# Performance work log

Measured on AMD Instinct MI355X. Metric: run time of the kernel, lower is better.

Reference implementation:

```python
import jax, jax.numpy as jnp
import numpy as np

N_NODES = 100000
IN_DIM = 64
HID = 64
N_EDGES = 1600000
EPS = 1e-5
SLOPE = 0.01  # F.leaky_relu default


def _glorot(key, shape):
    fan_in, fan_out = shape[1], shape[0]
    lim = jnp.sqrt(6.0 / (fan_in + fan_out))
    return jax.random.uniform(key, shape, jnp.float32, -lim, lim)


def setup_inputs() -> dict:
    key = jax.random.key(0)
    ks = jax.random.split(key, 8)
    x = jax.random.normal(ks[0], (N_NODES, IN_DIM), jnp.float32)
    src = jax.random.randint(ks[1], (N_EDGES,), 0, N_NODES, jnp.int32)
    dst = jax.random.randint(ks[2], (N_EDGES,), 0, N_NODES, jnp.int32)
    edge_index = jnp.stack([src, dst])  # [2, E]
    return {
        "x": x,
        "edge_index": edge_index,
        "W_self1": _glorot(ks[3], (HID, IN_DIM)),
        "W_neigh1": _glorot(ks[4], (HID, IN_DIM)),
        "b1": jnp.zeros((HID,), jnp.float32),
        "gamma1": jnp.ones((HID,), jnp.float32),
        "beta1": jnp.zeros((HID,), jnp.float32),
        "W_self2": _glorot(ks[5], (HID, HID)),
        "W_neigh2": _glorot(ks[6], (HID, HID)),
        "b2": jnp.zeros((HID,), jnp.float32),
        "gamma2": jnp.ones((HID,), jnp.float32),
        "beta2": jnp.zeros((HID,), jnp.float32),
    }


def _sage_mean(h, src, dst, W_self, W_neigh, b):
    # neighbor mean aggregation: mean of src features at each dst node
    msg_sum = jax.ops.segment_sum(h[src], dst, num_segments=N_NODES)  # [N, d]
    deg = jax.ops.segment_sum(jnp.ones_like(dst, jnp.float32), dst, num_segments=N_NODES)
    h_neigh = msg_sum / jnp.maximum(deg, 1.0)[:, None]  # isolated nodes -> 0
    return h @ W_self.T + h_neigh @ W_neigh.T + b


def _bn(h, gamma, beta):
    mu = jnp.mean(h, axis=0)
    var = jnp.mean(jnp.square(h - mu), axis=0)
    return (h - mu) * jax.lax.rsqrt(var + EPS) * gamma + beta


def reference(x, edge_index, W_self1, W_neigh1, b1, gamma1, beta1,
              W_self2, W_neigh2, b2, gamma2, beta2):
    src, dst = edge_index[0], edge_index[1]
    h = _sage_mean(x, src, dst, W_self1, W_neigh1, b1)
    h = jax.nn.leaky_relu(_bn(h, gamma1, beta1), SLOPE)
    h = _sage_mean(h, src, dst, W_self2, W_neigh2, b2)
    h = jax.nn.leaky_relu(_bn(h, gamma2, beta2), SLOPE)
    return h
```

## Files before the change

### kernel.cpp

```cpp
#include <hip/hip_runtime.h>

#define EPS 1e-5f
#define SLOPE 0.01f

typedef short bf16x8 __attribute__((ext_vector_type(8)));
typedef float f32x4 __attribute__((ext_vector_type(4)));

static __device__ __forceinline__ unsigned short f2bf(float f) {
  unsigned u = __float_as_uint(f);
  unsigned r = (u + 0x7FFFu + ((u >> 16) & 1u)) >> 16;
  return (unsigned short)r;
}
#define BFLO(u) __uint_as_float((u) << 16)
#define BFHI(u) __uint_as_float((u) & 0xFFFF0000u)


__global__ __launch_bounds__(1024) void hist_cvt_kernel(
    const int* __restrict__ dst, int* __restrict__ hist, int E, int NB,
    int histBlocks, const float* __restrict__ x, unsigned short* __restrict__ xb,
    int total4) {
  extern __shared__ int lh[];
  if ((int)blockIdx.x < histBlocks) {
    for (int i = threadIdx.x; i < NB; i += blockDim.x) lh[i] = 0;
    __syncthreads();
    int E4 = E >> 2;
    int stride = histBlocks * blockDim.x;
    const int4* d4 = (const int4*)dst;
    for (int i = blockIdx.x * blockDim.x + threadIdx.x; i < E4; i += stride) {
      int4 d = d4[i];
      atomicAdd(&lh[((unsigned)d.x) >> 8], 1);
      atomicAdd(&lh[((unsigned)d.y) >> 8], 1);
      atomicAdd(&lh[((unsigned)d.z) >> 8], 1);
      atomicAdd(&lh[((unsigned)d.w) >> 8], 1);
    }
    if (blockIdx.x == 0) {
      for (int i = (E4 << 2) + threadIdx.x; i < E; i += blockDim.x)
        atomicAdd(&lh[((unsigned)dst[i]) >> 8], 1);
    }
    __syncthreads();
    for (int b = threadIdx.x; b < NB; b += blockDim.x)
      hist[(size_t)b * histBlocks + blockIdx.x] = lh[b];
  } else {
    int cb = blockIdx.x - histBlocks;
    int stride = (gridDim.x - histBlocks) * blockDim.x;
    for (int i = cb * blockDim.x + threadIdx.x; i < total4; i += stride) {
      float4 v = reinterpret_cast<const float4*>(x)[i];
      ushort4 o;
      o.x = f2bf(v.x); o.y = f2bf(v.y); o.z = f2bf(v.z); o.w = f2bf(v.w);
      reinterpret_cast<ushort4*>(xb)[i] = o;
    }
  }
}

__global__ void scan_blk(const int* in, int* out, int* bsum, int n) {
  __shared__ int s[256];
  int i = blockIdx.x * 256 + threadIdx.x;
  int v = (i < n) ? in[i] : 0;
  s[threadIdx.x] = v;
  __syncthreads();
  for (int off = 1; off < 256; off <<= 1) {
    int t = (threadIdx.x >= off) ? s[threadIdx.x - off] : 0;
    __syncthreads();
    s[threadIdx.x] += t;
    __syncthreads();
  }
  if (i < n) out[i] = s[threadIdx.x] - v;
  if (threadIdx.x == 255) bsum[blockIdx.x] = s[255];
}

__global__ void scan_top(int* bsum, int nb) {
  __shared__ int s[512];
  int tid = threadIdx.x;
  int v = (tid < nb) ? bsum[tid] : 0;
  s[tid] = v;
  __syncthreads();
  for (int off = 1; off < 512; off <<= 1) {
    int t = (tid >= off) ? s[tid - off] : 0;
    __syncthreads();
    s[tid] += t;
    __syncthreads();
  }
  if (tid < nb) bsum[tid] = s[tid] - v;
}

__global__ __launch_bounds__(1024) void scatter_kernel(
    const int* __restrict__ src, const int* __restrict__ dst,
    const int* __restrict__ histS, const int* __restrict__ bsum,
    unsigned* __restrict__ binned, int E, int NB) {
  extern __shared__ int cur[];
  for (int b = threadIdx.x; b < NB; b += blockDim.x)
    cur[b] = histS[(size_t)b * gridDim.x + blockIdx.x] + bsum[b];
  __syncthreads();
  int E4 = E >> 2;
  int stride = gridDim.x * blockDim.x;
  const int4* d4 = (const int4*)dst;
  const int4* s4 = (const int4*)src;
  for (int i = blockIdx.x * blockDim.x + threadIdx.x; i < E4; i += stride) {
    int4 d = d4[i];
    int4 s = s4[i];
    int b0 = ((unsigned)d.x) >> 8;
    binned[atomicAdd(&cur[b0], 1)] = (unsigned)s.x | (((unsigned)d.x & 255u) << 20);
    int b1 = ((unsigned)d.y) >> 8;
    binned[atomicAdd(&cur[b1], 1)] = (unsigned)s.y | (((unsigned)d.y & 255u) << 20);
    int b2 = ((unsigned)d.z) >> 8;
    binned[atomicAdd(&cur[b2], 1)] = (unsigned)s.z | (((unsigned)d.z & 255u) << 20);
    int b3 = ((unsigned)d.w) >> 8;
    binned[atomicAdd(&cur[b3], 1)] = (unsigned)s.w | (((unsigned)d.w & 255u) << 20);
  }
  if (blockIdx.x == 0) {
    for (int i = (E4 << 2) + threadIdx.x; i < E; i += blockDim.x) {
      int d = dst[i];
      int b = ((unsigned)d) >> 8;
      binned[atomicAdd(&cur[b], 1)] = (unsigned)src[i] | (((unsigned)d & 255u) << 20);
    }
  }
}

__global__ __launch_bounds__(256) void fine_kernel(
    const unsigned* __restrict__ binned, const int* __restrict__ histS,
    const int* __restrict__ bsum,
    int* __restrict__ rowptr, int* __restrict__ col, int E, int NB, int NBLKB, int N) {
  __shared__ int ldeg[256];
  __shared__ int lcur[256];
  __shared__ int ss[256];
  int b = blockIdx.x;
  int tid = threadIdx.x;
  int seg_s = histS[(size_t)b * NBLKB] + bsum[b];
  int seg_e = (b + 1 < NB) ? (histS[(size_t)(b + 1) * NBLKB] + bsum[b + 1]) : E;
  ldeg[tid] = 0;
  __syncthreads();
  for (int i = seg_s + tid; i < seg_e; i += 256)
    atomicAdd(&ldeg[(binned[i] >> 20) & 255u], 1);
  __syncthreads();
  int d = ldeg[tid];
  ss[tid] = d;
  __syncthreads();
  for (int off = 1; off < 256; off <<= 1) {
    int t = (tid >= off) ? ss[tid - off] : 0;
    __syncthreads();
    ss[tid] += t;
    __syncthreads();
  }
  int base = seg_s + ss[tid] - d;
  lcur[tid] = base;
  int node = (b << 8) + tid;
  if (node < N) rowptr[node] = base;
  if (b == NB - 1 && tid == 0) rowptr[N] = E;
  __syncthreads();
  for (int i = seg_s + tid; i < seg_e; i += 256) {
    unsigned v = binned[i];
    int pos = atomicAdd(&lcur[(v >> 20) & 255u], 1);
    col[pos] = (int)(v & 0xFFFFFu);
  }
}


__global__ __launch_bounds__(256) void agg_kernel(
    const unsigned short* __restrict__ hb, const int* __restrict__ rowptr,
    const int* __restrict__ col, unsigned short* __restrict__ hm, int n) {
  int t = blockIdx.x * 256 + threadIdx.x;
  int node = t >> 3;
  int fo = (t & 7) * 8;
  if (node >= n) return;
  int beg = rowptr[node];
  int end = rowptr[node + 1];
  float s0 = 0.f, s1 = 0.f, s2 = 0.f, s3 = 0.f;
  float s4 = 0.f, s5 = 0.f, s6 = 0.f, s7 = 0.f;
  int e = beg;
  for (; e + 4 <= end; e += 4) {
    int i0 = col[e], i1 = col[e + 1], i2 = col[e + 2], i3 = col[e + 3];
    uint4 u0 = *reinterpret_cast<const uint4*>(&hb[(size_t)i0 * 64 + fo]);
    uint4 u1 = *reinterpret_cast<const uint4*>(&hb[(size_t)i1 * 64 + fo]);
    uint4 u2 = *reinterpret_cast<const uint4*>(&hb[(size_t)i2 * 64 + fo]);
    uint4 u3 = *reinterpret_cast<const uint4*>(&hb[(size_t)i3 * 64 + fo]);
    s0 += BFLO(u0.x) + BFLO(u1.x) + BFLO(u2.x) + BFLO(u3.x);
    s1 += BFHI(u0.x) + BFHI(u1.x) + BFHI(u2.x) + BFHI(u3.x);
    s2 += BFLO(u0.y) + BFLO(u1.y) + BFLO(u2.y) + BFLO(u3.y);
    s3 += BFHI(u0.y) + BFHI(u1.y) + BFHI(u2.y) + BFHI(u3.y);
    s4 += BFLO(u0.z) + BFLO(u1.z) + BFLO(u2.z) + BFLO(u3.z);
    s5 += BFHI(u0.z) + BFHI(u1.z) + BFHI(u2.z) + BFHI(u3.z);
    s6 += BFLO(u0.w) + BFLO(u1.w) + BFLO(u2.w) + BFLO(u3.w);
    s7 += BFHI(u0.w) + BFHI(u1.w) + BFHI(u2.w) + BFHI(u3.w);
  }
  for (; e < end; ++e) {
    uint4 u = *reinterpret_cast<const uint4*>(&hb[(size_t)col[e] * 64 + fo]);
    s0 += BFLO(u.x); s1 += BFHI(u.x);
    s2 += BFLO(u.y); s3 += BFHI(u.y);
    s4 += BFLO(u.z); s5 += BFHI(u.z);
    s6 += BFLO(u.w); s7 += BFHI(u.w);
  }
  int deg = end - beg;
  float inv = 1.0f / (float)(deg > 0 ? deg : 1);
  uint4 o;
  o.x = (unsigned)f2bf(s0 * inv) | ((unsigned)f2bf(s1 * inv) << 16);
  o.y = (unsigned)f2bf(s2 * inv) | ((unsigned)f2bf(s3 * inv) << 16);
  o.z = (unsigned)f2bf(s4 * inv) | ((unsigned)f2bf(s5 * inv) << 16);
  o.w = (unsigned)f2bf(s6 * inv) | ((unsigned)f2bf(s7 * inv) << 16);
  *reinterpret_cast<uint4*>(&hm[(size_t)node * 64 + fo]) = o;
}


__global__ __launch_bounds__(256) void gemm_stream(
    const unsigned short* __restrict__ A0,
    const unsigned short* __restrict__ A1,
    const float* __restrict__ Wself, const float* __restrict__ Wneigh,
    const float* __restrict__ bias,
    unsigned short* __restrict__ zb, float* __restrict__ partial, int n, int ntiles) {
  int tid = threadIdx.x;
  int lane = tid & 63;
  int w = tid >> 6;
  int l15 = lane & 15;
  int g = lane >> 4;

  bf16x8 B[4][4];
  #pragma unroll
  for (int t = 0; t < 4; ++t) {
    #pragma unroll
    for (int s = 0; s < 4; ++s) {
      const float* base = (s < 2 ? Wself : Wneigh) + (t * 16 + l15) * 64 + (s & 1) * 32 + g * 8;
      float4 w0 = *reinterpret_cast<const float4*>(base);
      float4 w1 = *reinterpret_cast<const float4*>(base + 4);
      bf16x8 b;
      b[0] = (short)f2bf(w0.x); b[1] = (short)f2bf(w0.y);
      b[2] = (short)f2bf(w0.z); b[3] = (short)f2bf(w0.w);
      b[4] = (short)f2bf(w1.x); b[5] = (short)f2bf(w1.y);
      b[6] = (short)f2bf(w1.z); b[7] = (short)f2bf(w1.w);
      B[t][s] = b;
    }
  }
  float bv[4];
  #pragma unroll
  for (int t = 0; t < 4; ++t) bv[t] = bias[t * 16 + l15];

  float ps[4] = {0.f, 0.f, 0.f, 0.f};
  float pq[4] = {0.f, 0.f, 0.f, 0.f};

  int nw = gridDim.x * 4;
  for (int tile = blockIdx.x * 4 + w; tile < ntiles; tile += nw) {
    int r0 = tile * 16 + l15;
    uint4 a[4];
    if (r0 < n) {
      const uint4* pa0 = reinterpret_cast<const uint4*>(A0 + (size_t)r0 * 64);
      const uint4* pa1 = reinterpret_cast<const uint4*>(A1 + (size_t)r0 * 64);
      a[0] = pa0[g]; a[1] = pa0[4 + g]; a[2] = pa1[g]; a[3] = pa1[4 + g];
    } else {
      a[0] = a[1] = a[2] = a[3] = make_uint4(0u, 0u, 0u, 0u);
    }
    f32x4 acc[4] = {};
    #pragma unroll
    for (int s = 0; s < 4; ++s) {
      bf16x8 af = *reinterpret_cast<bf16x8*>(&a[s]);
      #pragma unroll
      for (int t = 0; t < 4; ++t)
        acc[t] = __builtin_amdgcn_mfma_f32_16x16x32_bf16(af, B[t][s], acc[t], 0, 0, 0);
    }
    #pragma unroll
    for (int t = 0; t < 4; ++t) {
      #pragma unroll
      for (int i = 0; i < 4; ++i) {
        int gr = tile * 16 + g * 4 + i;
        if (gr < n) {
          float v = acc[t][i] + bv[t];
          zb[(size_t)gr * 64 + t * 16 + l15] = f2bf(v);
          ps[t] += v;
          pq[t] += v * v;
        }
      }
    }
  }

  #pragma unroll
  for (int t = 0; t < 4; ++t) {
    ps[t] += __shfl_xor(ps[t], 16); ps[t] += __shfl_xor(ps[t], 32);
    pq[t] += __shfl_xor(pq[t], 16); pq[t] += __shfl_xor(pq[t], 32);
  }
  __shared__ float sred[128];
  if (tid < 128) sred[tid] = 0.f;
  __syncthreads();
  if (lane < 16) {
    #pragma unroll
    for (int t = 0; t < 4; ++t) {
      atomicAdd(&sred[t * 16 + l15], ps[t]);
      atomicAdd(&sred[64 + t * 16 + l15], pq[t]);
    }
  }
  __syncthreads();
  if (tid < 128) partial[(size_t)blockIdx.x * 128 + tid] = sred[tid];
}

__global__ __launch_bounds__(256) void reduce_coef(
    const float* __restrict__ partial, const float* __restrict__ gamma,
    const float* __restrict__ beta, float* __restrict__ coef, int nblk, float invN) {
  int f = blockIdx.x;
  float s = 0.f, q = 0.f;
  for (int j = threadIdx.x; j < nblk; j += 256) {
    s += partial[(size_t)j * 128 + f];
    q += partial[(size_t)j * 128 + 64 + f];
  }
  #pragma unroll
  for (int o = 1; o < 64; o <<= 1) {
    s += __shfl_xor(s, o);
    q += __shfl_xor(q, o);
  }
  __shared__ float rs[4], rq[4];
  if ((threadIdx.x & 63) == 0) {
    rs[threadIdx.x >> 6] = s;
    rq[threadIdx.x >> 6] = q;
  }
  __syncthreads();
  if (threadIdx.x == 0) {
    float S = rs[0] + rs[1] + rs[2] + rs[3];
    float Q = rq[0] + rq[1] + rq[2] + rq[3];
    float mu = S * invN;
    float var = Q * invN - mu * mu;
    float sc = rsqrtf(var + EPS) * gamma[f];
    coef[f] = sc;
    coef[64 + f] = beta[f] - mu * sc;
  }
}


__global__ void bn_bf16_kernel(const unsigned short* __restrict__ zb,
                               const float* __restrict__ coef,
                               unsigned short* __restrict__ out, int n) {
  __shared__ float sc[64];
  __shared__ float sh[64];
  if (threadIdx.x < 64) {
    sc[threadIdx.x] = coef[threadIdx.x];
    sh[threadIdx.x] = coef[64 + threadIdx.x];
  }
  __syncthreads();
  int total = n * 16;
  int stride = gridDim.x * blockDim.x;
  for (int idx = blockIdx.x * blockDim.x + threadIdx.x; idx < total; idx += stride) {
    int f0 = (idx & 15) * 4;
    uint2 u = reinterpret_cast<const uint2*>(zb)[idx];
    float t;
    ushort4 o;
    t = BFLO(u.x) * sc[f0 + 0] + sh[f0 + 0]; o.x = f2bf(t > 0.f ? t : SLOPE * t);
    t = BFHI(u.x) * sc[f0 + 1] + sh[f0 + 1]; o.y = f2bf(t > 0.f ? t : SLOPE * t);
    t = BFLO(u.y) * sc[f0 + 2] + sh[f0 + 2]; o.z = f2bf(t > 0.f ? t : SLOPE * t);
    t = BFHI(u.y) * sc[f0 + 3] + sh[f0 + 3]; o.w = f2bf(t > 0.f ? t : SLOPE * t);
    reinterpret_cast<ushort4*>(out)[idx] = o;
  }
}

__global__ void bn_f32_kernel(const unsigned short* __restrict__ zb,
                              const float* __restrict__ coef,
                              float* __restrict__ out, int n) {
  __shared__ float sc[64];
  __shared__ float sh[64];
  if (threadIdx.x < 64) {
    sc[threadIdx.x] = coef[threadIdx.x];
    sh[threadIdx.x] = coef[64 + threadIdx.x];
  }
  __syncthreads();
  int total = n * 16;
  int stride = gridDim.x * blockDim.x;
  for (int idx = blockIdx.x * blockDim.x + threadIdx.x; idx < total; idx += stride) {
    int f0 = (idx & 15) * 4;
    uint2 u = reinterpret_cast<const uint2*>(zb)[idx];
    float4 o;
    float t;
    t = BFLO(u.x) * sc[f0 + 0] + sh[f0 + 0]; o.x = t > 0.f ? t : SLOPE * t;
    t = BFHI(u.x) * sc[f0 + 1] + sh[f0 + 1]; o.y = t > 0.f ? t : SLOPE * t;
    t = BFLO(u.y) * sc[f0 + 2] + sh[f0 + 2]; o.z = t > 0.f ? t : SLOPE * t;
    t = BFHI(u.y) * sc[f0 + 3] + sh[f0 + 3]; o.w = t > 0.f ? t : SLOPE * t;
    reinterpret_cast<float4*>(out)[idx] = o;
  }
}


extern "C" void kernel_launch(void* const* d_in, const int* in_sizes, int n_in,
                              void* d_out, int out_size, void* d_ws, size_t ws_size,
                              hipStream_t stream) {
  const float* x  = (const float*)d_in[0];
  const int* ei   = (const int*)d_in[1];
  const float* Ws1 = (const float*)d_in[2];
  const float* Wn1 = (const float*)d_in[3];
  const float* b1  = (const float*)d_in[4];
  const float* g1  = (const float*)d_in[5];
  const float* be1 = (const float*)d_in[6];
  const float* Ws2 = (const float*)d_in[7];
  const float* Wn2 = (const float*)d_in[8];
  const float* b2  = (const float*)d_in[9];
  const float* g2  = (const float*)d_in[10];
  const float* be2 = (const float*)d_in[11];
  float* out = (float*)d_out;

  int N = in_sizes[0] / 64;
  int E = in_sizes[1] / 2;
  const int* src = ei;
  const int* dst = ei + E;

  int NB = (N + 255) >> 8;
  const int NBLKB = 256;
  int M = NB * NBLKB;

  int ntiles = (N + 15) / 16;
  int gblk = (ntiles + 7) / 8;

  char* ws = (char*)d_ws;
  float* coef1 = (float*)ws;
  float* coef2 = coef1 + 128;
  size_t off = 1024;
  auto take = [&](size_t bytes) {
    void* p = ws + off;
    off = (off + bytes + 255) & ~(size_t)255;
    return p;
  };
  int* hist   = (int*)take((size_t)M * 4);
  int* bsum   = (int*)take(512 * 4);
  int* rowptr = (int*)take((size_t)(N + 1) * 4);
  unsigned* binned = (unsigned*)take((size_t)E * 4);
  int* col    = (int*)take((size_t)E * 4);
  unsigned short* xb  = (unsigned short*)take((size_t)N * 64 * 2);
  unsigned short* hmb = (unsigned short*)take((size_t)N * 64 * 2);
  unsigned short* h1b = (unsigned short*)take((size_t)N * 64 * 2);
  unsigned short* zb  = (unsigned short*)take((size_t)N * 64 * 2);
  float* partial = (float*)take((size_t)gblk * 128 * 4);

  hist_cvt_kernel<<<NBLKB + 128, 1024, NB * 4, stream>>>(dst, hist, E, NB, NBLKB,
                                                         x, xb, N * 16);
  int nb1 = (M + 255) / 256;
  scan_blk<<<nb1, 256, 0, stream>>>(hist, hist, bsum, M);
  scan_top<<<1, 512, 0, stream>>>(bsum, nb1);
  scatter_kernel<<<NBLKB, 1024, NB * 4, stream>>>(src, dst, hist, bsum, binned, E, NB);
  fine_kernel<<<NB, 256, 0, stream>>>(binned, hist, bsum, rowptr, col, E, NB, NBLKB, N);

  int ab = (N * 8 + 255) / 256;
  float invN = 1.0f / (float)N;

  agg_kernel<<<ab, 256, 0, stream>>>(xb, rowptr, col, hmb, N);
  gemm_stream<<<gblk, 256, 0, stream>>>(xb, hmb, Ws1, Wn1, b1, zb, partial, N, ntiles);
  reduce_coef<<<64, 256, 0, stream>>>(partial, g1, be1, coef1, gblk, invN);
  bn_bf16_kernel<<<2048, 256, 0, stream>>>(zb, coef1, h1b, N);

  agg_kernel<<<ab, 256, 0, stream>>>(h1b, rowptr, col, hmb, N);
  gemm_stream<<<gblk, 256, 0, stream>>>(h1b, hmb, Ws2, Wn2, b2, zb, partial, N, ntiles);
  reduce_coef<<<64, 256, 0, stream>>>(partial, g2, be2, coef2, gblk, invN);
  bn_f32_kernel<<<2048, 256, 0, stream>>>(zb, coef2, out, N);
}
```

Before: 174.8 us.

## Fuse neighbor aggregation into GEMM via shared-memory staging per 64-row tile

Merges the mean-aggregation kernel into the MFMA GEMM kernel. Each block of 256 threads now aggregates 64 nodes into an fp32 shared tile and converts it to bf16 MFMA operands directly. This removes the hmb intermediate buffer's write and reread plus one launch per layer. In exchange there are far more blocks (one per 64 rows), each reloading and converting the weights. The GEMM loses its persistent-tile loop, and the partial-stats array grows, which adds work to reduce_coef.

```diff
diff --git a/kernel.cpp b/kernel.cpp
--- a/kernel.cpp
+++ b/kernel.cpp
@@ -155,58 +155,63 @@
 }
 
 
-__global__ __launch_bounds__(256) void agg_kernel(
-    const unsigned short* __restrict__ hb, const int* __restrict__ rowptr,
-    const int* __restrict__ col, unsigned short* __restrict__ hm, int n) {
-  int t = blockIdx.x * 256 + threadIdx.x;
-  int node = t >> 3;
-  int fo = (t & 7) * 8;
-  if (node >= n) return;
-  int beg = rowptr[node];
-  int end = rowptr[node + 1];
-  float s0 = 0.f, s1 = 0.f, s2 = 0.f, s3 = 0.f;
-  float s4 = 0.f, s5 = 0.f, s6 = 0.f, s7 = 0.f;
-  int e = beg;
-  for (; e + 4 <= end; e += 4) {
-    int i0 = col[e], i1 = col[e + 1], i2 = col[e + 2], i3 = col[e + 3];
-    uint4 u0 = *reinterpret_cast<const uint4*>(&hb[(size_t)i0 * 64 + fo]);
-    uint4 u1 = *reinterpret_cast<const uint4*>(&hb[(size_t)i1 * 64 + fo]);
-    uint4 u2 = *reinterpret_cast<const uint4*>(&hb[(size_t)i2 * 64 + fo]);
-    uint4 u3 = *reinterpret_cast<const uint4*>(&hb[(size_t)i3 * 64 + fo]);
-    s0 += BFLO(u0.x) + BFLO(u1.x) + BFLO(u2.x) + BFLO(u3.x);
-    s1 += BFHI(u0.x) + BFHI(u1.x) + BFHI(u2.x) + BFHI(u3.x);
-    s2 += BFLO(u0.y) + BFLO(u1.y) + BFLO(u2.y) + BFLO(u3.y);
-    s3 += BFHI(u0.y) + BFHI(u1.y) + BFHI(u2.y) + BFHI(u3.y);
-    s4 += BFLO(u0.z) + BFLO(u1.z) + BFLO(u2.z) + BFLO(u3.z);
-    s5 += BFHI(u0.z) + BFHI(u1.z) + BFHI(u2.z) + BFHI(u3.z);
-    s6 += BFLO(u0.w) + BFLO(u1.w) + BFLO(u2.w) + BFLO(u3.w);
-    s7 += BFHI(u0.w) + BFHI(u1.w) + BFHI(u2.w) + BFHI(u3.w);
-  }
-  for (; e < end; ++e) {
-    uint4 u = *reinterpret_cast<const uint4*>(&hb[(size_t)col[e] * 64 + fo]);
-    s0 += BFLO(u.x); s1 += BFHI(u.x);
-    s2 += BFLO(u.y); s3 += BFHI(u.y);
-    s4 += BFLO(u.z); s5 += BFHI(u.z);
-    s6 += BFLO(u.w); s7 += BFHI(u.w);
-  }
-  int deg = end - beg;
-  float inv = 1.0f / (float)(deg > 0 ? deg : 1);
-  uint4 o;
-  o.x = (unsigned)f2bf(s0 * inv) | ((unsigned)f2bf(s1 * inv) << 16);
-  o.y = (unsigned)f2bf(s2 * inv) | ((unsigned)f2bf(s3 * inv) << 16);
-  o.z = (unsigned)f2bf(s4 * inv) | ((unsigned)f2bf(s5 * inv) << 16);
-  o.w = (unsigned)f2bf(s6 * inv) | ((unsigned)f2bf(s7 * inv) << 16);
-  *reinterpret_cast<uint4*>(&hm[(size_t)node * 64 + fo]) = o;
-}
-
-
-__global__ __launch_bounds__(256) void gemm_stream(
-    const unsigned short* __restrict__ A0,
-    const unsigned short* __restrict__ A1,
+#define XLD 65
+
+__global__ __launch_bounds__(256, 4) void fused_layer(
+    const unsigned short* __restrict__ hb,
+    const int* __restrict__ rowptr, const int* __restrict__ col,
     const float* __restrict__ Wself, const float* __restrict__ Wneigh,
     const float* __restrict__ bias,
-    unsigned short* __restrict__ zb, float* __restrict__ partial, int n, int ntiles) {
+    unsigned short* __restrict__ zb, float* __restrict__ partial, int n) {
+  __shared__ float X[64 * XLD];
+  __shared__ float sred[128];
   int tid = threadIdx.x;
+  int rowbase = blockIdx.x * 64;
+
+  int si = tid & 7;
+  int gi = tid >> 3;
+  #pragma unroll
+  for (int b = 0; b < 2; ++b) {
+    int node = rowbase + b * 32 + gi;
+    float a0 = 0.f, a1 = 0.f, a2 = 0.f, a3 = 0.f;
+    float a4 = 0.f, a5 = 0.f, a6 = 0.f, a7 = 0.f;
+    int deg = 0;
+    if (node < n) {
+      int beg = rowptr[node];
+      int end = rowptr[node + 1];
+      deg = end - beg;
+      int e = beg;
+      for (; e + 4 <= end; e += 4) {
+        int i0 = col[e], i1 = col[e + 1], i2 = col[e + 2], i3 = col[e + 3];
+        uint4 u0 = *reinterpret_cast<const uint4*>(&hb[(size_t)i0 * 64 + si * 8]);
+        uint4 u1 = *reinterpret_cast<const uint4*>(&hb[(size_t)i1 * 64 + si * 8]);
+        uint4 u2 = *reinterpret_cast<const uint4*>(&hb[(size_t)i2 * 64 + si * 8]);
+        uint4 u3 = *reinterpret_cast<const uint4*>(&hb[(size_t)i3 * 64 + si * 8]);
+        a0 += BFLO(u0.x) + BFLO(u1.x) + BFLO(u2.x) + BFLO(u3.x);
+        a1 += BFHI(u0.x) + BFHI(u1.x) + BFHI(u2.x) + BFHI(u3.x);
+        a2 += BFLO(u0.y) + BFLO(u1.y) + BFLO(u2.y) + BFLO(u3.y);
+        a3 += BFHI(u0.y) + BFHI(u1.y) + BFHI(u2.y) + BFHI(u3.y);
+        a4 += BFLO(u0.z) + BFLO(u1.z) + BFLO(u2.z) + BFLO(u3.z);
+        a5 += BFHI(u0.z) + BFHI(u1.z) + BFHI(u2.z) + BFHI(u3.z);
+        a6 += BFLO(u0.w) + BFLO(u1.w) + BFLO(u2.w) + BFLO(u3.w);
+        a7 += BFHI(u0.w) + BFHI(u1.w) + BFHI(u2.w) + BFHI(u3.w);
+      }
+      for (; e < end; ++e) {
+        uint4 u = *reinterpret_cast<const uint4*>(&hb[(size_t)col[e] * 64 + si * 8]);
+        a0 += BFLO(u.x); a1 += BFHI(u.x);
+        a2 += BFLO(u.y); a3 += BFHI(u.y);
+        a4 += BFLO(u.z); a5 += BFHI(u.z);
+        a6 += BFLO(u.w); a7 += BFHI(u.w);
+      }
+    }
+    float inv = 1.0f / (float)(deg > 0 ? deg : 1);
+    float* xr = &X[(b * 32 + gi) * XLD + si * 8];
+    xr[0] = a0 * inv; xr[1] = a1 * inv; xr[2] = a2 * inv; xr[3] = a3 * inv;
+    xr[4] = a4 * inv; xr[5] = a5 * inv; xr[6] = a6 * inv; xr[7] = a7 * inv;
+  }
+  if (tid < 128) sred[tid] = 0.f;
+  __syncthreads();
+
   int lane = tid & 63;
   int w = tid >> 6;
   int l15 = lane & 15;
@@ -220,51 +225,59 @@
       const float* base = (s < 2 ? Wself : Wneigh) + (t * 16 + l15) * 64 + (s & 1) * 32 + g * 8;
       float4 w0 = *reinterpret_cast<const float4*>(base);
       float4 w1 = *reinterpret_cast<const float4*>(base + 4);
-      bf16x8 b;
-      b[0] = (short)f2bf(w0.x); b[1] = (short)f2bf(w0.y);
-      b[2] = (short)f2bf(w0.z); b[3] = (short)f2bf(w0.w);
-      b[4] = (short)f2bf(w1.x); b[5] = (short)f2bf(w1.y);
-      b[6] = (short)f2bf(w1.z); b[7] = (short)f2bf(w1.w);
-      B[t][s] = b;
+      bf16x8 bb;
+      bb[0] = (short)f2bf(w0.x); bb[1] = (short)f2bf(w0.y);
+      bb[2] = (short)f2bf(w0.z); bb[3] = (short)f2bf(w0.w);
+      bb[4] = (short)f2bf(w1.x); bb[5] = (short)f2bf(w1.y);
+      bb[6] = (short)f2bf(w1.z); bb[7] = (short)f2bf(w1.w);
+      B[t][s] = bb;
     }
   }
   float bv[4];
   #pragma unroll
   for (int t = 0; t < 4; ++t) bv[t] = bias[t * 16 + l15];
+
+  int r0 = rowbase + w * 16 + l15;
+  uint4 a0[2];
+  if (r0 < n) {
+    const uint4* pa0 = reinterpret_cast<const uint4*>(hb + (size_t)r0 * 64);
+    a0[0] = pa0[g]; a0[1] = pa0[4 + g];
+  } else {
+    a0[0] = a0[1] = make_uint4(0u, 0u, 0u, 0u);
+  }
+  const float* xr = &X[(w * 16 + l15) * XLD];
+  bf16x8 a1[2];
+  #pragma unroll
+  for (int h = 0; h < 2; ++h) {
+    const float* p = xr + h * 32 + g * 8;
+    bf16x8 v;
+    #pragma unroll
+    for (int j = 0; j < 8; ++j) v[j] = (short)f2bf(p[j]);
+    a1[h] = v;
+  }
+
+  f32x4 acc[4] = {};
+  #pragma unroll
+  for (int s = 0; s < 4; ++s) {
+    bf16x8 af = (s < 2) ? *reinterpret_cast<bf16x8*>(&a0[s])
+                        : a1[s - 2];
+    #pragma unroll
+    for (int t = 0; t < 4; ++t)
+      acc[t] = __builtin_amdgcn_mfma_f32_16x16x32_bf16(af, B[t][s], acc[t], 0, 0, 0);
+  }
 
   float ps[4] = {0.f, 0.f, 0.f, 0.f};
   float pq[4] = {0.f, 0.f, 0.f, 0.f};
-
-  int nw = gridDim.x * 4;
-  for (int tile = blockIdx.x * 4 + w; tile < ntiles; tile += nw) {
-    int r0 = tile * 16 + l15;
-    uint4 a[4];
-    if (r0 < n) {
-      const uint4* pa0 = reinterpret_cast<const uint4*>(A0 + (size_t)r0 * 64);
-      const uint4* pa1 = reinterpret_cast<const uint4*>(A1 + (size_t)r0 * 64);
-      a[0] = pa0[g]; a[1] = pa0[4 + g]; a[2] = pa1[g]; a[3] = pa1[4 + g];
-    } else {
-      a[0] = a[1] = a[2] = a[3] = make_uint4(0u, 0u, 0u, 0u);
-    }
-    f32x4 acc[4] = {};
+  #pragma unroll
+  for (int t = 0; t < 4; ++t) {
     #pragma unroll
-    for (int s = 0; s < 4; ++s) {
-      bf16x8 af = *reinterpret_cast<bf16x8*>(&a[s]);
-      #pragma unroll
-      for (int t = 0; t < 4; ++t)
-        acc[t] = __builtin_amdgcn_mfma_f32_16x16x32_bf16(af, B[t][s], acc[t], 0, 0, 0);
-    }
-    #pragma unroll
-    for (int t = 0; t < 4; ++t) {
-      #pragma unroll
-      for (int i = 0; i < 4; ++i) {
-        int gr = tile * 16 + g * 4 + i;
-        if (gr < n) {
-          float v = acc[t][i] + bv[t];
-          zb[(size_t)gr * 64 + t * 16 + l15] = f2bf(v);
-          ps[t] += v;
-          pq[t] += v * v;
-        }
+    for (int i = 0; i < 4; ++i) {
+      int gr = rowbase + w * 16 + g * 4 + i;
+      if (gr < n) {
+        float v = acc[t][i] + bv[t];
+        zb[(size_t)gr * 64 + t * 16 + l15] = f2bf(v);
+        ps[t] += v;
+        pq[t] += v * v;
       }
     }
   }
@@ -274,9 +287,6 @@
     ps[t] += __shfl_xor(ps[t], 16); ps[t] += __shfl_xor(ps[t], 32);
     pq[t] += __shfl_xor(pq[t], 16); pq[t] += __shfl_xor(pq[t], 32);
   }
-  __shared__ float sred[128];
-  if (tid < 128) sred[tid] = 0.f;
-  __syncthreads();
   if (lane < 16) {
     #pragma unroll
     for (int t = 0; t < 4; ++t) {
@@ -397,8 +407,7 @@
   const int NBLKB = 256;
   int M = NB * NBLKB;
 
-  int ntiles = (N + 15) / 16;
-  int gblk = (ntiles + 7) / 8;
+  int NSUPER = (N + 63) / 64;
 
   char* ws = (char*)d_ws;
   float* coef1 = (float*)ws;
@@ -415,10 +424,9 @@
   unsigned* binned = (unsigned*)take((size_t)E * 4);
   int* col    = (int*)take((size_t)E * 4);
   unsigned short* xb  = (unsigned short*)take((size_t)N * 64 * 2);
-  unsigned short* hmb = (unsigned short*)take((size_t)N * 64 * 2);
   unsigned short* h1b = (unsigned short*)take((size_t)N * 64 * 2);
   unsigned short* zb  = (unsigned short*)take((size_t)N * 64 * 2);
-  float* partial = (float*)take((size_t)gblk * 128 * 4);
+  float* partial = (float*)take((size_t)NSUPER * 128 * 4);
 
   hist_cvt_kernel<<<NBLKB + 128, 1024, NB * 4, stream>>>(dst, hist, E, NB, NBLKB,
                                                          x, xb, N * 16);
@@ -428,16 +436,13 @@
   scatter_kernel<<<NBLKB, 1024, NB * 4, stream>>>(src, dst, hist, bsum, binned, E, NB);
   fine_kernel<<<NB, 256, 0, stream>>>(binned, hist, bsum, rowptr, col, E, NB, NBLKB, N);
 
-  int ab = (N * 8 + 255) / 256;
   float invN = 1.0f / (float)N;
 
-  agg_kernel<<<ab, 256, 0, stream>>>(xb, rowptr, col, hmb, N);
-  gemm_stream<<<gblk, 256, 0, stream>>>(xb, hmb, Ws1, Wn1, b1, zb, partial, N, ntiles);
-  reduce_coef<<<64, 256, 0, stream>>>(partial, g1, be1, coef1, gblk, invN);
+  fused_layer<<<NSUPER, 256, 0, stream>>>(xb, rowptr, col, Ws1, Wn1, b1, zb, partial, N);
+  reduce_coef<<<64, 256, 0, stream>>>(partial, g1, be1, coef1, NSUPER, invN);
   bn_bf16_kernel<<<2048, 256, 0, stream>>>(zb, coef1, h1b, N);
 
-  agg_kernel<<<ab, 256, 0, stream>>>(h1b, rowptr, col, hmb, N);
-  gemm_stream<<<gblk, 256, 0, stream>>>(h1b, hmb, Ws2, Wn2, b2, zb, partial, N, ntiles);
-  reduce_coef<<<64, 256, 0, stream>>>(partial, g2, be2, coef2, gblk, invN);
+  fused_layer<<<NSUPER, 256, 0, stream>>>(h1b, rowptr, col, Ws2, Wn2, b2, zb, partial, N);
+  reduce_coef<<<64, 256, 0, stream>>>(partial, g2, be2, coef2, NSUPER, invN);
   bn_f32_kernel<<<2048, 256, 0, stream>>>(zb, coef2, out, N);
 }
```

Measured after the change: 244.3 us. 39.8% more time.

## Fuse layer-1 batchnorm and leaky ReLU into layer-2 aggregation and GEMM

Applied to the files above, without the earlier changes.

Removes the standalone bf16 batchnorm pass for layer 1 and its intermediate h1b buffer. The layer-1 BN scale/shift and leaky ReLU are now applied on the fly to the raw pre-BN activations: per gathered neighbour row in the aggregation kernel, and per self row in the GEMM kernel. This saves one full read and write of the N×64 activation array plus a kernel launch. In exchange the aggregation does extra FMA and select work for every edge. The GEMM also reads and writes zb in place, which conflicts with its __restrict__ qualifiers. An occupancy hint (launch_bounds 256,8) is also added to the aggregation kernel.

```diff
diff --git a/kernel.cpp b/kernel.cpp
--- a/kernel.cpp
+++ b/kernel.cpp
@@ -155,17 +155,43 @@
 }
 
 
-__global__ __launch_bounds__(256) void agg_kernel(
+template <bool BN>
+__global__ __launch_bounds__(256, 8) void agg_kernel(
     const unsigned short* __restrict__ hb, const int* __restrict__ rowptr,
-    const int* __restrict__ col, unsigned short* __restrict__ hm, int n) {
+    const int* __restrict__ col, const float* __restrict__ coef,
+    unsigned short* __restrict__ hm, int n) {
   int t = blockIdx.x * 256 + threadIdx.x;
   int node = t >> 3;
   int fo = (t & 7) * 8;
   if (node >= n) return;
+  float scr[8], shr[8];
+  if (BN) {
+    #pragma unroll
+    for (int j = 0; j < 8; ++j) {
+      scr[j] = coef[fo + j];
+      shr[j] = coef[64 + fo + j];
+    }
+  }
   int beg = rowptr[node];
   int end = rowptr[node + 1];
   float s0 = 0.f, s1 = 0.f, s2 = 0.f, s3 = 0.f;
   float s4 = 0.f, s5 = 0.f, s6 = 0.f, s7 = 0.f;
+  auto acc1 = [&](uint4 u) {
+    float v0 = BFLO(u.x), v1 = BFHI(u.x), v2 = BFLO(u.y), v3 = BFHI(u.y);
+    float v4 = BFLO(u.z), v5 = BFHI(u.z), v6 = BFLO(u.w), v7 = BFHI(u.w);
+    if (BN) {
+      v0 = v0 * scr[0] + shr[0]; v0 = v0 > 0.f ? v0 : SLOPE * v0;
+      v1 = v1 * scr[1] + shr[1]; v1 = v1 > 0.f ? v1 : SLOPE * v1;
+      v2 = v2 * scr[2] + shr[2]; v2 = v2 > 0.f ? v2 : SLOPE * v2;
+      v3 = v3 * scr[3] + shr[3]; v3 = v3 > 0.f ? v3 : SLOPE * v3;
+      v4 = v4 * scr[4] + shr[4]; v4 = v4 > 0.f ? v4 : SLOPE * v4;
+      v5 = v5 * scr[5] + shr[5]; v5 = v5 > 0.f ? v5 : SLOPE * v5;
+      v6 = v6 * scr[6] + shr[6]; v6 = v6 > 0.f ? v6 : SLOPE * v6;
+      v7 = v7 * scr[7] + shr[7]; v7 = v7 > 0.f ? v7 : SLOPE * v7;
+    }
+    s0 += v0; s1 += v1; s2 += v2; s3 += v3;
+    s4 += v4; s5 += v5; s6 += v6; s7 += v7;
+  };
   int e = beg;
   for (; e + 4 <= end; e += 4) {
     int i0 = col[e], i1 = col[e + 1], i2 = col[e + 2], i3 = col[e + 3];
@@ -173,21 +199,11 @@
     uint4 u1 = *reinterpret_cast<const uint4*>(&hb[(size_t)i1 * 64 + fo]);
     uint4 u2 = *reinterpret_cast<const uint4*>(&hb[(size_t)i2 * 64 + fo]);
     uint4 u3 = *reinterpret_cast<const uint4*>(&hb[(size_t)i3 * 64 + fo]);
-    s0 += BFLO(u0.x) + BFLO(u1.x) + BFLO(u2.x) + BFLO(u3.x);
-    s1 += BFHI(u0.x) + BFHI(u1.x) + BFHI(u2.x) + BFHI(u3.x);
-    s2 += BFLO(u0.y) + BFLO(u1.y) + BFLO(u2.y) + BFLO(u3.y);
-    s3 += BFHI(u0.y) + BFHI(u1.y) + BFHI(u2.y) + BFHI(u3.y);
-    s4 += BFLO(u0.z) + BFLO(u1.z) + BFLO(u2.z) + BFLO(u3.z);
-    s5 += BFHI(u0.z) + BFHI(u1.z) + BFHI(u2.z) + BFHI(u3.z);
-    s6 += BFLO(u0.w) + BFLO(u1.w) + BFLO(u2.w) + BFLO(u3.w);
-    s7 += BFHI(u0.w) + BFHI(u1.w) + BFHI(u2.w) + BFHI(u3.w);
+    acc1(u0); acc1(u1); acc1(u2); acc1(u3);
   }
   for (; e < end; ++e) {
     uint4 u = *reinterpret_cast<const uint4*>(&hb[(size_t)col[e] * 64 + fo]);
-    s0 += BFLO(u.x); s1 += BFHI(u.x);
-    s2 += BFLO(u.y); s3 += BFHI(u.y);
-    s4 += BFLO(u.z); s5 += BFHI(u.z);
-    s6 += BFLO(u.w); s7 += BFHI(u.w);
+    acc1(u);
   }
   int deg = end - beg;
   float inv = 1.0f / (float)(deg > 0 ? deg : 1);
@@ -200,11 +216,12 @@
 }
 
 
+template <bool BN>
 __global__ __launch_bounds__(256) void gemm_stream(
     const unsigned short* __restrict__ A0,
     const unsigned short* __restrict__ A1,
     const float* __restrict__ Wself, const float* __restrict__ Wneigh,
-    const float* __restrict__ bias,
+    const float* __restrict__ bias, const float* __restrict__ coef,
     unsigned short* __restrict__ zb, float* __restrict__ partial, int n, int ntiles) {
   int tid = threadIdx.x;
   int lane = tid & 63;
@@ -232,6 +249,18 @@
   #pragma unroll
   for (int t = 0; t < 4; ++t) bv[t] = bias[t * 16 + l15];
 
+  float scA[2][8], shA[2][8];
+  if (BN) {
+    #pragma unroll
+    for (int h = 0; h < 2; ++h) {
+      #pragma unroll
+      for (int j = 0; j < 8; ++j) {
+        scA[h][j] = coef[h * 32 + g * 8 + j];
+        shA[h][j] = coef[64 + h * 32 + g * 8 + j];
+      }
+    }
+  }
+
   float ps[4] = {0.f, 0.f, 0.f, 0.f};
   float pq[4] = {0.f, 0.f, 0.f, 0.f};
 
@@ -245,6 +274,28 @@
       a[0] = pa0[g]; a[1] = pa0[4 + g]; a[2] = pa1[g]; a[3] = pa1[4 + g];
     } else {
       a[0] = a[1] = a[2] = a[3] = make_uint4(0u, 0u, 0u, 0u);
+    }
+    if (BN) {
+      #pragma unroll
+      for (int h = 0; h < 2; ++h) {
+        uint4 u = a[h];
+        float v0 = BFLO(u.x), v1 = BFHI(u.x), v2 = BFLO(u.y), v3 = BFHI(u.y);
+        float v4 = BFLO(u.z), v5 = BFHI(u.z), v6 = BFLO(u.w), v7 = BFHI(u.w);
+        v0 = v0 * scA[h][0] + shA[h][0]; v0 = v0 > 0.f ? v0 : SLOPE * v0;
+        v1 = v1 * scA[h][1] + shA[h][1]; v1 = v1 > 0.f ? v1 : SLOPE * v1;
+        v2 = v2 * scA[h][2] + shA[h][2]; v2 = v2 > 0.f ? v2 : SLOPE * v2;
+        v3 = v3 * scA[h][3] + shA[h][3]; v3 = v3 > 0.f ? v3 : SLOPE * v3;
+        v4 = v4 * scA[h][4] + shA[h][4]; v4 = v4 > 0.f ? v4 : SLOPE * v4;
+        v5 = v5 * scA[h][5] + shA[h][5]; v5 = v5 > 0.f ? v5 : SLOPE * v5;
+        v6 = v6 * scA[h][6] + shA[h][6]; v6 = v6 > 0.f ? v6 : SLOPE * v6;
+        v7 = v7 * scA[h][7] + shA[h][7]; v7 = v7 > 0.f ? v7 : SLOPE * v7;
+        uint4 r;
+        r.x = (unsigned)f2bf(v0) | ((unsigned)f2bf(v1) << 16);
+        r.y = (unsigned)f2bf(v2) | ((unsigned)f2bf(v3) << 16);
+        r.z = (unsigned)f2bf(v4) | ((unsigned)f2bf(v5) << 16);
+        r.w = (unsigned)f2bf(v6) | ((unsigned)f2bf(v7) << 16);
+        a[h] = r;
+      }
     }
     f32x4 acc[4] = {};
     #pragma unroll
@@ -319,31 +370,6 @@
   }
 }
 
-
-__global__ void bn_bf16_kernel(const unsigned short* __restrict__ zb,
-                               const float* __restrict__ coef,
-                               unsigned short* __restrict__ out, int n) {
-  __shared__ float sc[64];
-  __shared__ float sh[64];
-  if (threadIdx.x < 64) {
-    sc[threadIdx.x] = coef[threadIdx.x];
-    sh[threadIdx.x] = coef[64 + threadIdx.x];
-  }
-  __syncthreads();
-  int total = n * 16;
-  int stride = gridDim.x * blockDim.x;
-  for (int idx = blockIdx.x * blockDim.x + threadIdx.x; idx < total; idx += stride) {
-    int f0 = (idx & 15) * 4;
-    uint2 u = reinterpret_cast<const uint2*>(zb)[idx];
-    float t;
-    ushort4 o;
-    t = BFLO(u.x) * sc[f0 + 0] + sh[f0 + 0]; o.x = f2bf(t > 0.f ? t : SLOPE * t);
-    t = BFHI(u.x) * sc[f0 + 1] + sh[f0 + 1]; o.y = f2bf(t > 0.f ? t : SLOPE * t);
-    t = BFLO(u.y) * sc[f0 + 2] + sh[f0 + 2]; o.z = f2bf(t > 0.f ? t : SLOPE * t);
-    t = BFHI(u.y) * sc[f0 + 3] + sh[f0 + 3]; o.w = f2bf(t > 0.f ? t : SLOPE * t);
-    reinterpret_cast<ushort4*>(out)[idx] = o;
-  }
-}
 
 __global__ void bn_f32_kernel(const unsigned short* __restrict__ zb,
                               const float* __restrict__ coef,
@@ -416,7 +442,6 @@
   int* col    = (int*)take((size_t)E * 4);
   unsigned short* xb  = (unsigned short*)take((size_t)N * 64 * 2);
   unsigned short* hmb = (unsigned short*)take((size_t)N * 64 * 2);
-  unsigned short* h1b = (unsigned short*)take((size_t)N * 64 * 2);
   unsigned short* zb  = (unsigned short*)take((size_t)N * 64 * 2);
   float* partial = (float*)take((size_t)gblk * 128 * 4);
 
@@ -431,13 +456,14 @@
   int ab = (N * 8 + 255) / 256;
   float invN = 1.0f / (float)N;
 
-  agg_kernel<<<ab, 256, 0, stream>>>(xb, rowptr, col, hmb, N);
-  gemm_stream<<<gblk, 256, 0, stream>>>(xb, hmb, Ws1, Wn1, b1, zb, partial, N, ntiles);
+  agg_kernel<false><<<ab, 256, 0, stream>>>(xb, rowptr, col, nullptr, hmb, N);
+  gemm_stream<false><<<gblk, 256, 0, stream>>>(xb, hmb, Ws1, Wn1, b1, nullptr,
+                                               zb, partial, N, ntiles);
   reduce_coef<<<64, 256, 0, stream>>>(partial, g1, be1, coef1, gblk, invN);
-  bn_bf16_kernel<<<2048, 256, 0, stream>>>(zb, coef1, h1b, N);
-
-  agg_kernel<<<ab, 256, 0, stream>>>(h1b, rowptr, col, hmb, N);
-  gemm_stream<<<gblk, 256, 0, stream>>>(h1b, hmb, Ws2, Wn2, b2, zb, partial, N, ntiles);
+
+  agg_kernel<true><<<ab, 256, 0, stream>>>(zb, rowptr, col, coef1, hmb, N);
+  gemm_stream<true><<<gblk, 256, 0, stream>>>(zb, hmb, Ws2, Wn2, b2, coef1,
+                                              zb, partial, N, ntiles);
   reduce_coef<<<64, 256, 0, stream>>>(partial, g2, be2, coef2, gblk, invN);
   bn_f32_kernel<<<2048, 256, 0, stream>>>(zb, coef2, out, N);
 }
```

Result: slower. 182.4 us (+4.4%).

## Pad CSR rows to multiples of four with dummy zero node for vector index loads

Applied to the files above, without the earlier changes.

Each node's adjacency list is padded to a multiple of four entries and filled with a sentinel index pointing to an extra all-zero feature row. The aggregation kernel can then load column indices as int4 and drop the scalar tail loop. The CSR changes from rowptr to separate degree and start-pointer arrays. In exchange the col array grows, extra gathers read the zero row, and two small memsets are added.

```diff
diff --git a/kernel.cpp b/kernel.cpp
--- a/kernel.cpp
+++ b/kernel.cpp
@@ -119,7 +119,8 @@
 __global__ __launch_bounds__(256) void fine_kernel(
     const unsigned* __restrict__ binned, const int* __restrict__ histS,
     const int* __restrict__ bsum,
-    int* __restrict__ rowptr, int* __restrict__ col, int E, int NB, int NBLKB, int N) {
+    int* __restrict__ degarr, int* __restrict__ pptr, int* __restrict__ col,
+    int E, int NB, int NBLKB, int N) {
   __shared__ int ldeg[256];
   __shared__ int lcur[256];
   __shared__ int ss[256];
@@ -127,13 +128,15 @@
   int tid = threadIdx.x;
   int seg_s = histS[(size_t)b * NBLKB] + bsum[b];
   int seg_e = (b + 1 < NB) ? (histS[(size_t)(b + 1) * NBLKB] + bsum[b + 1]) : E;
+  int pbase = (seg_s + b * 1024 + 3) & ~3;
   ldeg[tid] = 0;
   __syncthreads();
   for (int i = seg_s + tid; i < seg_e; i += 256)
     atomicAdd(&ldeg[(binned[i] >> 20) & 255u], 1);
   __syncthreads();
   int d = ldeg[tid];
-  ss[tid] = d;
+  int pd = (d + 3) & ~3;
+  ss[tid] = pd;
   __syncthreads();
   for (int off = 1; off < 256; off <<= 1) {
     int t = (tid >= off) ? ss[tid - off] : 0;
@@ -141,38 +144,42 @@
     ss[tid] += t;
     __syncthreads();
   }
-  int base = seg_s + ss[tid] - d;
-  lcur[tid] = base;
+  int pstart = pbase + ss[tid] - pd;
+  lcur[tid] = pstart;
   int node = (b << 8) + tid;
-  if (node < N) rowptr[node] = base;
-  if (b == NB - 1 && tid == 0) rowptr[N] = E;
+  if (node < N) {
+    degarr[node] = d;
+    pptr[node] = pstart;
+  }
   __syncthreads();
   for (int i = seg_s + tid; i < seg_e; i += 256) {
     unsigned v = binned[i];
     int pos = atomicAdd(&lcur[(v >> 20) & 255u], 1);
     col[pos] = (int)(v & 0xFFFFFu);
   }
+  for (int k = d; k < pd; ++k) col[pstart + k] = N;
 }
 
 
 __global__ __launch_bounds__(256) void agg_kernel(
-    const unsigned short* __restrict__ hb, const int* __restrict__ rowptr,
-    const int* __restrict__ col, unsigned short* __restrict__ hm, int n) {
+    const unsigned short* __restrict__ hb, const int* __restrict__ degarr,
+    const int* __restrict__ pptr, const int* __restrict__ col,
+    unsigned short* __restrict__ hm, int n) {
   int t = blockIdx.x * 256 + threadIdx.x;
   int node = t >> 3;
   int fo = (t & 7) * 8;
   if (node >= n) return;
-  int beg = rowptr[node];
-  int end = rowptr[node + 1];
+  int deg = degarr[node];
+  const int4* cp = reinterpret_cast<const int4*>(col + pptr[node]);
+  int nit = (deg + 3) >> 2;
   float s0 = 0.f, s1 = 0.f, s2 = 0.f, s3 = 0.f;
   float s4 = 0.f, s5 = 0.f, s6 = 0.f, s7 = 0.f;
-  int e = beg;
-  for (; e + 4 <= end; e += 4) {
-    int i0 = col[e], i1 = col[e + 1], i2 = col[e + 2], i3 = col[e + 3];
-    uint4 u0 = *reinterpret_cast<const uint4*>(&hb[(size_t)i0 * 64 + fo]);
-    uint4 u1 = *reinterpret_cast<const uint4*>(&hb[(size_t)i1 * 64 + fo]);
-    uint4 u2 = *reinterpret_cast<const uint4*>(&hb[(size_t)i2 * 64 + fo]);
-    uint4 u3 = *reinterpret_cast<const uint4*>(&hb[(size_t)i3 * 64 + fo]);
+  for (int it = 0; it < nit; ++it) {
+    int4 c = cp[it];
+    uint4 u0 = *reinterpret_cast<const uint4*>(&hb[(size_t)c.x * 64 + fo]);
+    uint4 u1 = *reinterpret_cast<const uint4*>(&hb[(size_t)c.y * 64 + fo]);
+    uint4 u2 = *reinterpret_cast<const uint4*>(&hb[(size_t)c.z * 64 + fo]);
+    uint4 u3 = *reinterpret_cast<const uint4*>(&hb[(size_t)c.w * 64 + fo]);
     s0 += BFLO(u0.x) + BFLO(u1.x) + BFLO(u2.x) + BFLO(u3.x);
     s1 += BFHI(u0.x) + BFHI(u1.x) + BFHI(u2.x) + BFHI(u3.x);
     s2 += BFLO(u0.y) + BFLO(u1.y) + BFLO(u2.y) + BFLO(u3.y);
@@ -182,14 +189,6 @@
     s6 += BFLO(u0.w) + BFLO(u1.w) + BFLO(u2.w) + BFLO(u3.w);
     s7 += BFHI(u0.w) + BFHI(u1.w) + BFHI(u2.w) + BFHI(u3.w);
   }
-  for (; e < end; ++e) {
-    uint4 u = *reinterpret_cast<const uint4*>(&hb[(size_t)col[e] * 64 + fo]);
-    s0 += BFLO(u.x); s1 += BFHI(u.x);
-    s2 += BFLO(u.y); s3 += BFHI(u.y);
-    s4 += BFLO(u.z); s5 += BFHI(u.z);
-    s6 += BFLO(u.w); s7 += BFHI(u.w);
-  }
-  int deg = end - beg;
   float inv = 1.0f / (float)(deg > 0 ? deg : 1);
   uint4 o;
   o.x = (unsigned)f2bf(s0 * inv) | ((unsigned)f2bf(s1 * inv) << 16);
@@ -411,14 +410,18 @@
   };
   int* hist   = (int*)take((size_t)M * 4);
   int* bsum   = (int*)take(512 * 4);
-  int* rowptr = (int*)take((size_t)(N + 1) * 4);
+  int* degarr = (int*)take((size_t)N * 4);
+  int* pptr   = (int*)take((size_t)N * 4);
   unsigned* binned = (unsigned*)take((size_t)E * 4);
-  int* col    = (int*)take((size_t)E * 4);
-  unsigned short* xb  = (unsigned short*)take((size_t)N * 64 * 2);
+  int* col    = (int*)take(((size_t)E + (size_t)NB * 1024 + 1024) * 4);
+  unsigned short* xb  = (unsigned short*)take((size_t)(N + 1) * 64 * 2);
   unsigned short* hmb = (unsigned short*)take((size_t)N * 64 * 2);
-  unsigned short* h1b = (unsigned short*)take((size_t)N * 64 * 2);
+  unsigned short* h1b = (unsigned short*)take((size_t)(N + 1) * 64 * 2);
   unsigned short* zb  = (unsigned short*)take((size_t)N * 64 * 2);
   float* partial = (float*)take((size_t)gblk * 128 * 4);
+
+  hipMemsetAsync(xb + (size_t)N * 64, 0, 128, stream);
+  hipMemsetAsync(h1b + (size_t)N * 64, 0, 128, stream);
 
   hist_cvt_kernel<<<NBLKB + 128, 1024, NB * 4, stream>>>(dst, hist, E, NB, NBLKB,
                                                          x, xb, N * 16);
@@ -426,17 +429,18 @@
   scan_blk<<<nb1, 256, 0, stream>>>(hist, hist, bsum, M);
   scan_top<<<1, 512, 0, stream>>>(bsum, nb1);
   scatter_kernel<<<NBLKB, 1024, NB * 4, stream>>>(src, dst, hist, bsum, binned, E, NB);
-  fine_kernel<<<NB, 256, 0, stream>>>(binned, hist, bsum, rowptr, col, E, NB, NBLKB, N);
+  fine_kernel<<<NB, 256, 0, stream>>>(binned, hist, bsum, degarr, pptr, col,
+                                      E, NB, NBLKB, N);
 
   int ab = (N * 8 + 255) / 256;
   float invN = 1.0f / (float)N;
 
-  agg_kernel<<<ab, 256, 0, stream>>>(xb, rowptr, col, hmb, N);
+  agg_kernel<<<ab, 256, 0, stream>>>(xb, degarr, pptr, col, hmb, N);
   gemm_stream<<<gblk, 256, 0, stream>>>(xb, hmb, Ws1, Wn1, b1, zb, partial, N, ntiles);
   reduce_coef<<<64, 256, 0, stream>>>(partial, g1, be1, coef1, gblk, invN);
   bn_bf16_kernel<<<2048, 256, 0, stream>>>(zb, coef1, h1b, N);
 
-  agg_kernel<<<ab, 256, 0, stream>>>(h1b, rowptr, col, hmb, N);
+  agg_kernel<<<ab, 256, 0, stream>>>(h1b, degarr, pptr, col, hmb, N);
   gemm_stream<<<gblk, 256, 0, stream>>>(h1b, hmb, Ws2, Wn2, b2, zb, partial, N, ntiles);
   reduce_coef<<<64, 256, 0, stream>>>(partial, g2, be2, coef2, gblk, invN);
   bn_f32_kernel<<<2048, 256, 0, stream>>>(zb, coef2, out, N);
```

New measurement: 180.6 us. 1.03x slower.
